# Kernel tuning notes

Hardware: AMD Instinct MI355X
Metric: run time of the kernel (lower is better)

Reference implementation:

```python
import jax, jax.numpy as jnp
import numpy as np

B, T, D, H = 8, 2048, 1024, 128  # batch, seq, input_size, head_size


def setup_inputs() -> dict:
    key = jax.random.key(0)
    kx, kq, kk, kv = jax.random.split(key, 4)
    s = 1.0 / np.sqrt(D)
    return {
        "x": jax.random.normal(kx, (B, T, D), dtype=jnp.float32),
        "Wq": jax.random.normal(kq, (D, H), dtype=jnp.float32) * s,
        "Wk": jax.random.normal(kk, (D, H), dtype=jnp.float32) * s,
        "Wv": jax.random.normal(kv, (D, H), dtype=jnp.float32) * s,
    }


def reference(x, Wq, Wk, Wv):
    # projections (Linear, no bias)
    q = jnp.einsum("btd,dh->bth", x, Wq)
    k = jnp.einsum("btd,dh->bth", x, Wk)
    v = jnp.einsum("btd,dh->bth", x, Wv)
    scale = H ** (-0.5)
    scores = jnp.einsum("bth,bsh->bts", q, k) * scale  # [B,T,T]
    t = x.shape[1]
    causal = jnp.tril(jnp.ones((t, t), dtype=bool))
    scores = jnp.where(causal, scores, -jnp.inf)
    attn = jax.nn.softmax(scores, axis=-1)  # dropout p=0.0 -> identity
    out = jnp.einsum("bts,bsh->bth", attn, v)
    return out
```

## Files before the change

### kernel.cpp

```cpp
#include <hip/hip_runtime.h>
#include <math.h>

#define B_ 8
#define T_ 2048
#define D_ 1024
#define H_ 128
#define BT (B_ * T_)

typedef short bf16x8 __attribute__((ext_vector_type(8)));
typedef float f32x4 __attribute__((ext_vector_type(4)));

static constexpr float SCALE = 0.08838834764831845f;
static constexpr float SCALE2 = 0.127517416f;

__device__ inline unsigned short f2b(float f) {
  unsigned int u = __float_as_uint(f);
  u += 0x7FFF + ((u >> 16) & 1);
  return (unsigned short)(u >> 16);
}
__device__ inline unsigned int pk2(float a, float b) {
  return (unsigned int)f2b(a) | ((unsigned int)f2b(b) << 16);
}

__device__ __forceinline__ void gll16(const void* g, void* l) {
  __builtin_amdgcn_global_load_lds(
      (const __attribute__((address_space(1))) void*)g,
      (__attribute__((address_space(3))) void*)l, 16, 0, 0);
}

__global__ __launch_bounds__(256) void wcvt_kernel(
    const float* __restrict__ Wq, const float* __restrict__ Wk,
    const float* __restrict__ Wv, short* __restrict__ Wt) {
  __shared__ short Wls[128 * 72];
  const int sel = blockIdx.y;
  const float* W = sel == 0 ? Wq : (sel == 1 ? Wk : Wv);
  const int d0 = blockIdx.x * 64;
  const int tid = threadIdx.x;
#pragma unroll
  for (int i = 0; i < 8; ++i) {
    int slot = tid + i * 256;
    int r = slot >> 5, hg = slot & 31;
    float4 w = *(const float4*)(W + (size_t)(d0 + r) * H_ + hg * 4);
    Wls[(hg * 4 + 0) * 72 + r] = (short)f2b(w.x);
    Wls[(hg * 4 + 1) * 72 + r] = (short)f2b(w.y);
    Wls[(hg * 4 + 2) * 72 + r] = (short)f2b(w.z);
    Wls[(hg * 4 + 3) * 72 + r] = (short)f2b(w.w);
  }
  __syncthreads();
  short* dst = Wt + (size_t)sel * D_ * H_;
#pragma unroll
  for (int i = 0; i < 4; ++i) {
    int slot = tid + i * 256;
    int h = slot >> 3, g = slot & 7;
    *(int4*)(dst + (size_t)h * D_ + d0 + g * 8) = *(int4*)&Wls[h * 72 + g * 8];
  }
}

__global__ __launch_bounds__(256) void proj_kernel(
    const float* __restrict__ x, const short* __restrict__ Wt,
    short* __restrict__ qb, short* __restrict__ kb, short* __restrict__ vtb) {
  __shared__ alignas(16) char smem[49152];
  short* Xs0 = (short*)smem;
  short* Xs1 = (short*)(smem + 8192);
  short* Ws0 = (short*)(smem + 16384);
  short* Ws1 = (short*)(smem + 32768);

  const int tid = threadIdx.x;
  const int wave = tid >> 6, lane = tid & 63;
  const int ln = lane & 15, quad = lane >> 4;
  const int mw = wave & 1, nw = wave >> 1;
  const int sel = blockIdx.y;
  const int row0 = blockIdx.x * 64;
  const short* W = Wt + (size_t)sel * (size_t)(D_ * H_);

  f32x4 acc[2][4];
#pragma unroll
  for (int mi = 0; mi < 2; ++mi)
#pragma unroll
    for (int ni = 0; ni < 4; ++ni) acc[mi][ni] = (f32x4){0.f, 0.f, 0.f, 0.f};

  auto stageW = [&](int bf, int k0) {
    short* Ws = bf ? Ws1 : Ws0;
#pragma unroll
    for (int j = 0; j < 4; ++j) {
      const int rbase = wave * 32 + j * 8;
      const int n = rbase + (lane >> 3);
      const int gp = (lane & 7) ^ (n & 7);
      gll16(W + (size_t)n * D_ + k0 + gp * 8, (char*)Ws + rbase * 128);
    }
  };
  auto packX = [&](int bf, const float4* xr) {
    short* Xs = bf ? Xs1 : Xs0;
#pragma unroll
    for (int i = 0; i < 4; ++i) {
      int fid = tid + i * 256;
      int r = fid >> 4, g4 = fid & 15;
      int g = g4 >> 1, half = g4 & 1;
      unsigned int* p = (unsigned int*)&Xs[r * 64 + ((g ^ (r & 7)) * 8) + half * 4];
      p[0] = pk2(xr[i].x, xr[i].y);
      p[1] = pk2(xr[i].z, xr[i].w);
    }
  };

  {
    stageW(0, 0);
    float4 xr[4];
#pragma unroll
    for (int i = 0; i < 4; ++i) {
      int fid = tid + i * 256;
      int r = fid >> 4, g4 = fid & 15;
      xr[i] = *(const float4*)(x + (size_t)(row0 + r) * D_ + g4 * 4);
    }
    packX(0, xr);
  }

  for (int s = 0; s < 16; ++s) {
    __syncthreads();
    float4 xr[4];
    const bool pre = (s < 15);
    if (pre) {
      const int k0n = (s + 1) * 64;
      stageW((s + 1) & 1, k0n);
#pragma unroll
      for (int i = 0; i < 4; ++i) {
        int fid = tid + i * 256;
        int r = fid >> 4, g4 = fid & 15;
        xr[i] = *(const float4*)(x + (size_t)(row0 + r) * D_ + k0n + g4 * 4);
      }
    }
    const short* Xs = (s & 1) ? Xs1 : Xs0;
    const short* Ws = (s & 1) ? Ws1 : Ws0;
#pragma unroll
    for (int kk = 0; kk < 2; ++kk) {
      bf16x8 a[2];
#pragma unroll
      for (int mi = 0; mi < 2; ++mi) {
        int r = mw * 32 + mi * 16 + ln;
        a[mi] = *(bf16x8*)&Xs[r * 64 + (((kk * 4 + quad) ^ (r & 7)) * 8)];
      }
#pragma unroll
      for (int ni = 0; ni < 4; ++ni) {
        int n = nw * 64 + ni * 16 + ln;
        bf16x8 bb = *(bf16x8*)&Ws[n * 64 + (((kk * 4 + quad) ^ (n & 7)) * 8)];
#pragma unroll
        for (int mi = 0; mi < 2; ++mi)
          acc[mi][ni] = __builtin_amdgcn_mfma_f32_16x16x32_bf16(a[mi], bb, acc[mi][ni], 0, 0, 0);
      }
    }
    if (pre) packX((s + 1) & 1, xr);
  }

  __syncthreads();
  short* Cs = (short*)smem;
  if (sel < 2) {
    short* out = sel ? kb : qb;
#pragma unroll
    for (int mi = 0; mi < 2; ++mi)
#pragma unroll
      for (int ni = 0; ni < 4; ++ni)
#pragma unroll
        for (int rr = 0; rr < 4; ++rr)
          Cs[(mw * 32 + mi * 16 + quad * 4 + rr) * 136 + nw * 64 + ni * 16 + ln] =
              (short)f2b(acc[mi][ni][rr]);
    __syncthreads();
#pragma unroll
    for (int i = 0; i < 4; ++i) {
      int slot = tid + i * 256;
      int r = slot >> 4, g = slot & 15;
      *(int4*)(out + (size_t)(row0 + r) * H_ + g * 8) = *(int4*)&Cs[r * 136 + g * 8];
    }
  } else {
#pragma unroll
    for (int mi = 0; mi < 2; ++mi)
#pragma unroll
      for (int ni = 0; ni < 4; ++ni)
#pragma unroll
        for (int rr = 0; rr < 4; ++rr)
          Cs[(nw * 64 + ni * 16 + ln) * 72 + mw * 32 + mi * 16 + quad * 4 + rr] =
              (short)f2b(acc[mi][ni][rr]);
    __syncthreads();
    const int b = row0 >> 11, t0 = row0 & 2047;
#pragma unroll
    for (int i = 0; i < 4; ++i) {
      int slot = tid + i * 256;
      int h = slot >> 3, g = slot & 7;
      *(int4*)(vtb + (size_t)(b * H_ + h) * T_ + t0 + g * 8) = *(int4*)&Cs[h * 72 + g * 8];
    }
  }
}

__global__ __launch_bounds__(256) void attn_part(
    const short* __restrict__ qb, const short* __restrict__ kb,
    const short* __restrict__ vtb, float* __restrict__ po,
    float* __restrict__ pm, float* __restrict__ pl) {
  __shared__ alignas(16) char smem[74240];
  short* Ks0 = (short*)smem;
  short* Ks1 = (short*)(smem + 16384);
  short* Vt0 = (short*)(smem + 32768);
  short* Vt1 = (short*)(smem + 49152);
  short* Pt  = (short*)(smem + 65536);

  const int tid = threadIdx.x;
  const int wv = tid >> 6, lane = tid & 63;
  const int ln = lane & 15, quad = lane >> 4;
  const int b = blockIdx.x / 40;
  const int rr = 39 - (blockIdx.x % 40);
  const int G = (rr >= 24) ? 3 : (rr >= 12) ? 2 : (rr >= 4) ? 1 : 0;
  const int local = rr - 2 * G * (G + 1);
  const int j = 4 * G + local / (G + 1);
  const int s = local - (local / (G + 1)) * (G + 1);
  const int sid = b * 40 + rr;
  const int q0 = j * 128;
  const int nchunks = min(8, 2 * j + 2 - 8 * s);

  short* myP = Pt + wv * (16 * 68);

  bf16x8 qfr[2][4];
#pragma unroll
  for (int m = 0; m < 2; ++m)
#pragma unroll
    for (int kk = 0; kk < 4; ++kk)
      qfr[m][kk] = *(const bf16x8*)(qb +
          (size_t)(b * T_ + q0 + wv * 32 + m * 16 + ln) * H_ + kk * 32 + quad * 8);

  f32x4 oacc[2][8];
#pragma unroll
  for (int m = 0; m < 2; ++m)
#pragma unroll
    for (int ht = 0; ht < 8; ++ht) oacc[m][ht] = (f32x4){0.f, 0.f, 0.f, 0.f};

  float m_run[2] = {-INFINITY, -INFINITY};
  float l_run[2] = {0.f, 0.f};

  auto stageK = [&](short* dst, int s0) {
#pragma unroll
    for (int jj = 0; jj < 4; ++jj) {
      const int rb = wv * 16 + jj * 4;
      const int r = rb + (lane >> 4);
      const int gp = (lane & 15) ^ (r & 7);
      gll16(kb + (size_t)(b * T_ + s0 + r) * H_ + gp * 8, (char*)dst + rb * 256);
    }
  };
  auto stageV = [&](short* dst, int s0) {
#pragma unroll
    for (int jj = 0; jj < 4; ++jj) {
      const int hb = wv * 32 + jj * 8;
      const int h = hb + (lane >> 3);
      const int gp = (lane & 7) ^ (h & 7);
      gll16(vtb + (size_t)(b * H_ + h) * T_ + s0 + gp * 8, (char*)dst + hb * 128);
    }
  };

  stageK(Ks0, 8 * s * 64);
  stageV(Vt0, 8 * s * 64);

  for (int ch = 0; ch < nchunks; ++ch) {
    const int s0 = (8 * s + ch) * 64;
    const int cur = ch & 1;
    __syncthreads();
    if (ch + 1 < nchunks) {
      stageK(cur ? Ks0 : Ks1, s0 + 64);
      stageV(cur ? Vt0 : Vt1, s0 + 64);
    }
    const short* Kc = cur ? Ks1 : Ks0;
    const short* Vc = cur ? Vt1 : Vt0;

    f32x4 sacc[2][4];
#pragma unroll
    for (int m = 0; m < 2; ++m)
#pragma unroll
      for (int t = 0; t < 4; ++t) sacc[m][t] = (f32x4){0.f, 0.f, 0.f, 0.f};
#pragma unroll
    for (int kk = 0; kk < 4; ++kk) {
#pragma unroll
      for (int t = 0; t < 4; ++t) {
        const int krow = t * 16 + ln;
        bf16x8 kf = *(bf16x8*)&Kc[krow * 128 + (((kk * 4 + quad) ^ (ln & 7)) * 8)];
#pragma unroll
        for (int m = 0; m < 2; ++m)
          sacc[m][t] = __builtin_amdgcn_mfma_f32_16x16x32_bf16(kf, qfr[m][kk], sacc[m][t], 0, 0, 0);
      }
    }

    const bool needMask = (s0 + 63 > q0 + wv * 32);
    float p[2][4][4], alpha[2];
#pragma unroll
    for (int m = 0; m < 2; ++m) {
      const int qg = q0 + wv * 32 + m * 16 + ln;
      float sv[4][4];
      float mc = -INFINITY;
#pragma unroll
      for (int t = 0; t < 4; ++t)
#pragma unroll
        for (int r = 0; r < 4; ++r) {
          float scv = sacc[m][t][r] * SCALE2;
          if (needMask) {
            const int key = s0 + t * 16 + quad * 4 + r;
            scv = (key <= qg) ? scv : -INFINITY;
          }
          sv[t][r] = scv;
          mc = fmaxf(mc, scv);
        }
      mc = fmaxf(mc, __shfl_xor(mc, 16));
      mc = fmaxf(mc, __shfl_xor(mc, 32));
      const float mnew = fmaxf(m_run[m], mc);
      alpha[m] = exp2f(m_run[m] - mnew);
      float lc = 0.f;
#pragma unroll
      for (int t = 0; t < 4; ++t)
#pragma unroll
        for (int r = 0; r < 4; ++r) {
          p[m][t][r] = exp2f(sv[t][r] - mnew);
          lc += p[m][t][r];
        }
      lc += __shfl_xor(lc, 16);
      lc += __shfl_xor(lc, 32);
      l_run[m] = l_run[m] * alpha[m] + lc;
      m_run[m] = mnew;
    }

#pragma unroll
    for (int m = 0; m < 2; ++m) {
#pragma unroll
      for (int ht = 0; ht < 8; ++ht)
#pragma unroll
        for (int r = 0; r < 4; ++r) oacc[m][ht][r] *= alpha[m];
#pragma unroll
      for (int t = 0; t < 4; ++t) {
        *(unsigned int*)&myP[ln * 68 + t * 16 + quad * 4 + 0] = pk2(p[m][t][0], p[m][t][1]);
        *(unsigned int*)&myP[ln * 68 + t * 16 + quad * 4 + 2] = pk2(p[m][t][2], p[m][t][3]);
      }
#pragma unroll
      for (int kk2 = 0; kk2 < 2; ++kk2) {
        bf16x8 pf = *(bf16x8*)&myP[ln * 68 + kk2 * 32 + quad * 8];
#pragma unroll
        for (int ht = 0; ht < 8; ++ht) {
          const int hrow = ht * 16 + ln;
          bf16x8 vf = *(bf16x8*)&Vc[hrow * 64 + (((kk2 * 4 + quad) ^ (ln & 7)) * 8)];
          oacc[m][ht] = __builtin_amdgcn_mfma_f32_16x16x32_bf16(vf, pf, oacc[m][ht], 0, 0, 0);
        }
      }
    }
  }

  if (quad == 0) {
#pragma unroll
    for (int m = 0; m < 2; ++m) {
      pm[(size_t)sid * 128 + wv * 32 + m * 16 + ln] = m_run[m];
      pl[(size_t)sid * 128 + wv * 32 + m * 16 + ln] = l_run[m];
    }
  }
  __syncthreads();
  float* Ot = (float*)smem;
#pragma unroll
  for (int m = 0; m < 2; ++m)
#pragma unroll
    for (int ht = 0; ht < 8; ++ht)
      *(f32x4*)&Ot[(wv * 32 + m * 16 + ln) * 132 + ht * 16 + quad * 4] = oacc[m][ht];
  __syncthreads();
  float* dst = po + (size_t)sid * 16384;
#pragma unroll
  for (int i = 0; i < 16; ++i) {
    int slot2 = tid + i * 256;
    int r2 = slot2 >> 5, c2 = slot2 & 31;
    *(f32x4*)(dst + r2 * 128 + c2 * 4) = *(f32x4*)&Ot[r2 * 132 + c2 * 4];
  }
}

__global__ __launch_bounds__(256) void attn_reduce(
    const float* __restrict__ po, const float* __restrict__ pm,
    const float* __restrict__ pl, float* __restrict__ out) {
  const int b = blockIdx.x >> 5;
  const int rem = blockIdx.x & 31;
  const int j = rem >> 1, half = rem & 1;
  const int G = j >> 2;
  const int nseg = G + 1;
  const int sid0 = b * 40 + 2 * G * (G + 1) + (j - 4 * G) * nseg;
  const int tid = threadIdx.x;
  const int q = half * 64 + (tid >> 2), hq = tid & 3;

  float m2[4], l[4], a[4];
  float M2 = -INFINITY;
  for (int s2 = 0; s2 < nseg; ++s2) {
    m2[s2] = pm[(size_t)(sid0 + s2) * 128 + q];
    l[s2] = pl[(size_t)(sid0 + s2) * 128 + q];
    M2 = fmaxf(M2, m2[s2]);
  }
  float lsum = 0.f;
  for (int s2 = 0; s2 < nseg; ++s2) {
    a[s2] = exp2f(m2[s2] - M2);
    lsum += a[s2] * l[s2];
  }
  f32x4 acc[8];
#pragma unroll
  for (int i = 0; i < 8; ++i) acc[i] = (f32x4){0.f, 0.f, 0.f, 0.f};
  for (int s2 = 0; s2 < nseg; ++s2) {
    const float* src = po + (size_t)(sid0 + s2) * 16384 + q * 128 + hq * 32;
    const float as = a[s2];
#pragma unroll
    for (int i = 0; i < 8; ++i) {
      f32x4 v = *(const f32x4*)(src + i * 4);
#pragma unroll
      for (int c = 0; c < 4; ++c) acc[i][c] += as * v[c];
    }
  }
  const float inv = 1.0f / lsum;
  float* o = out + ((size_t)(b * T_ + j * 128 + q)) * H_ + hq * 32;
#pragma unroll
  for (int i = 0; i < 8; ++i) {
    f32x4 v;
#pragma unroll
    for (int c = 0; c < 4; ++c) v[c] = acc[i][c] * inv;
    *(f32x4*)(o + i * 4) = v;
  }
}

extern "C" void kernel_launch(void* const* d_in, const int* in_sizes, int n_in,
                              void* d_out, int out_size, void* d_ws, size_t ws_size,
                              hipStream_t stream) {
  const float* x  = (const float*)d_in[0];
  const float* Wq = (const float*)d_in[1];
  const float* Wk = (const float*)d_in[2];
  const float* Wv = (const float*)d_in[3];
  float* out = (float*)d_out;

  char* ws = (char*)d_ws;
  short* qb  = (short*)(ws);
  short* kb  = (short*)(ws + 4194304);
  short* vtb = (short*)(ws + 8388608);
  short* Wt  = (short*)(ws + 12582912);
  float* po  = (float*)(ws + 14680064);
  float* pm  = (float*)(ws + 35651584);
  float* pl  = (float*)(ws + 35915776);

  wcvt_kernel<<<dim3(D_ / 64, 3), 256, 0, stream>>>(Wq, Wk, Wv, Wt);
  proj_kernel<<<dim3(BT / 64, 3), 256, 0, stream>>>(x, Wt, qb, kb, vtb);
  attn_part<<<dim3(8 * 40), 256, 0, stream>>>(qb, kb, vtb, po, pm, pl);
  attn_reduce<<<dim3(8 * 32), 256, 0, stream>>>(po, pm, pl, out);
}
```

Baseline: 172.7 us.

## Split causal attention into finer KV segments and store partials as bf16

Changes the split-KV partition so each block handles at most 4 KV chunks (256 keys) instead of 8, which raises the grid from 320 to 576 blocks and evens out per-block work. The partial outputs are now written as bf16 rather than fp32, halving partial-output traffic, and the reduce kernel merges up to 8 segments. The costs are more partial segments for the reduce to combine, more repeated Q loads, and reduced precision in the partial accumulators.

After: 183.1 us. 6.0% more time.

```diff
diff --git a/kernel.cpp b/kernel.cpp
--- a/kernel.cpp
+++ b/kernel.cpp
@@ -10,7 +10,6 @@
 typedef short bf16x8 __attribute__((ext_vector_type(8)));
 typedef float f32x4 __attribute__((ext_vector_type(4)));
 
-static constexpr float SCALE = 0.08838834764831845f;
 static constexpr float SCALE2 = 0.127517416f;
 
 __device__ inline unsigned short f2b(float f) {
@@ -20,6 +19,9 @@
 }
 __device__ inline unsigned int pk2(float a, float b) {
   return (unsigned int)f2b(a) | ((unsigned int)f2b(b) << 16);
+}
+__device__ inline float b2f(unsigned short u) {
+  return __uint_as_float((unsigned int)u << 16);
 }
 
 __device__ __forceinline__ void gll16(const void* g, void* l) {
@@ -191,7 +193,7 @@
 
 __global__ __launch_bounds__(256) void attn_part(
     const short* __restrict__ qb, const short* __restrict__ kb,
-    const short* __restrict__ vtb, float* __restrict__ po,
+    const short* __restrict__ vtb, short* __restrict__ po,
     float* __restrict__ pm, float* __restrict__ pl) {
   __shared__ alignas(16) char smem[74240];
   short* Ks0 = (short*)smem;
@@ -203,15 +205,16 @@
   const int tid = threadIdx.x;
   const int wv = tid >> 6, lane = tid & 63;
   const int ln = lane & 15, quad = lane >> 4;
-  const int b = blockIdx.x / 40;
-  const int rr = 39 - (blockIdx.x % 40);
-  const int G = (rr >= 24) ? 3 : (rr >= 12) ? 2 : (rr >= 4) ? 1 : 0;
-  const int local = rr - 2 * G * (G + 1);
-  const int j = 4 * G + local / (G + 1);
-  const int s = local - (local / (G + 1)) * (G + 1);
-  const int sid = b * 40 + rr;
+  const int b = blockIdx.x / 72;
+  const int rr = 71 - (blockIdx.x % 72);
+  int a = 0;
+  while ((a + 1) * (a + 2) <= rr) ++a;
+  const int local = rr - a * (a + 1);
+  const int j = 2 * a + local / (a + 1);
+  const int s = local % (a + 1);
+  const int sid = b * 72 + rr;
   const int q0 = j * 128;
-  const int nchunks = min(8, 2 * j + 2 - 8 * s);
+  const int nchunks = min(4, 2 * j + 2 - 4 * s);
 
   short* myP = Pt + wv * (16 * 68);
 
@@ -251,11 +254,11 @@
     }
   };
 
-  stageK(Ks0, 8 * s * 64);
-  stageV(Vt0, 8 * s * 64);
+  stageK(Ks0, 4 * s * 64);
+  stageV(Vt0, 4 * s * 64);
 
   for (int ch = 0; ch < nchunks; ++ch) {
-    const int s0 = (8 * s + ch) * 64;
+    const int s0 = (4 * s + ch) * 64;
     const int cur = ch & 1;
     __syncthreads();
     if (ch + 1 < nchunks) {
@@ -358,28 +361,32 @@
     for (int ht = 0; ht < 8; ++ht)
       *(f32x4*)&Ot[(wv * 32 + m * 16 + ln) * 132 + ht * 16 + quad * 4] = oacc[m][ht];
   __syncthreads();
-  float* dst = po + (size_t)sid * 16384;
+  short* dst = po + (size_t)sid * 16384;
 #pragma unroll
   for (int i = 0; i < 16; ++i) {
     int slot2 = tid + i * 256;
     int r2 = slot2 >> 5, c2 = slot2 & 31;
-    *(f32x4*)(dst + r2 * 128 + c2 * 4) = *(f32x4*)&Ot[r2 * 132 + c2 * 4];
+    f32x4 v = *(f32x4*)&Ot[r2 * 132 + c2 * 4];
+    int2 w2;
+    w2.x = (int)pk2(v[0], v[1]);
+    w2.y = (int)pk2(v[2], v[3]);
+    *(int2*)(dst + r2 * 128 + c2 * 4) = w2;
   }
 }
 
 __global__ __launch_bounds__(256) void attn_reduce(
-    const float* __restrict__ po, const float* __restrict__ pm,
+    const short* __restrict__ po, const float* __restrict__ pm,
     const float* __restrict__ pl, float* __restrict__ out) {
   const int b = blockIdx.x >> 5;
   const int rem = blockIdx.x & 31;
   const int j = rem >> 1, half = rem & 1;
-  const int G = j >> 2;
-  const int nseg = G + 1;
-  const int sid0 = b * 40 + 2 * G * (G + 1) + (j - 4 * G) * nseg;
+  const int a = j >> 1;
+  const int nseg = a + 1;
+  const int sid0 = b * 72 + a * (a + 1) + (j - 2 * a) * (a + 1);
   const int tid = threadIdx.x;
   const int q = half * 64 + (tid >> 2), hq = tid & 3;
 
-  float m2[4], l[4], a[4];
+  float m2[8], l[8], w[8];
   float M2 = -INFINITY;
   for (int s2 = 0; s2 < nseg; ++s2) {
     m2[s2] = pm[(size_t)(sid0 + s2) * 128 + q];
@@ -388,20 +395,25 @@
   }
   float lsum = 0.f;
   for (int s2 = 0; s2 < nseg; ++s2) {
-    a[s2] = exp2f(m2[s2] - M2);
-    lsum += a[s2] * l[s2];
+    w[s2] = exp2f(m2[s2] - M2);
+    lsum += w[s2] * l[s2];
   }
   f32x4 acc[8];
 #pragma unroll
   for (int i = 0; i < 8; ++i) acc[i] = (f32x4){0.f, 0.f, 0.f, 0.f};
   for (int s2 = 0; s2 < nseg; ++s2) {
-    const float* src = po + (size_t)(sid0 + s2) * 16384 + q * 128 + hq * 32;
-    const float as = a[s2];
-#pragma unroll
-    for (int i = 0; i < 8; ++i) {
-      f32x4 v = *(const f32x4*)(src + i * 4);
-#pragma unroll
-      for (int c = 0; c < 4; ++c) acc[i][c] += as * v[c];
+    const short* src = po + (size_t)(sid0 + s2) * 16384 + q * 128 + hq * 32;
+    const float as = w[s2];
+#pragma unroll
+    for (int i = 0; i < 4; ++i) {
+      int4 v = *(const int4*)(src + i * 8);
+      const unsigned int* pu = (const unsigned int*)&v;
+#pragma unroll
+      for (int c = 0; c < 4; ++c) {
+        unsigned int u = pu[c];
+        acc[i * 2 + (c >> 1)][(c & 1) * 2 + 0] += as * b2f((unsigned short)(u & 0xFFFF));
+        acc[i * 2 + (c >> 1)][(c & 1) * 2 + 1] += as * b2f((unsigned short)(u >> 16));
+      }
     }
   }
   const float inv = 1.0f / lsum;
@@ -429,12 +441,12 @@
   short* kb  = (short*)(ws + 4194304);
   short* vtb = (short*)(ws + 8388608);
   short* Wt  = (short*)(ws + 12582912);
-  float* po  = (float*)(ws + 14680064);
-  float* pm  = (float*)(ws + 35651584);
-  float* pl  = (float*)(ws + 35915776);
+  short* po  = (short*)(ws + 14680064);
+  float* pm  = (float*)(ws + 33554432);
+  float* pl  = (float*)(ws + 33849344);
 
   wcvt_kernel<<<dim3(D_ / 64, 3), 256, 0, stream>>>(Wq, Wk, Wv, Wt);
   proj_kernel<<<dim3(BT / 64, 3), 256, 0, stream>>>(x, Wt, qb, kb, vtb);
-  attn_part<<<dim3(8 * 40), 256, 0, stream>>>(qb, kb, vtb, po, pm, pl);
+  attn_part<<<dim3(8 * 72), 256, 0, stream>>>(qb, kb, vtb, po, pm, pl);
   attn_reduce<<<dim3(8 * 32), 256, 0, stream>>>(po, pm, pl, out);
 }
```
